# Kernel optimization log

Hardware: AMD Instinct MI355X
Metric: run time of the kernel (lower is better)

The kernel has to match this reference:

```python
import jax, jax.numpy as jnp
import numpy as np

B, N, D, H, FF = 4, 1024, 512, 8, 2048
DH = D // H
RPE_HID = 16
COORD_DIM = 2


def _ln(x, g, b, eps=1e-5):
    m = jnp.mean(x, axis=-1, keepdims=True)
    v = jnp.mean((x - m) ** 2, axis=-1, keepdims=True)
    return (x - m) * jax.lax.rsqrt(v + eps) * g + b


def setup_inputs() -> dict:
    key = jax.random.key(0)
    ks = jax.random.split(key, 20)
    s = 0.02
    inp = {
        "x": jax.random.normal(ks[0], (B, N, D), dtype=jnp.float32),
        "coords": jax.random.uniform(ks[1], (B, N, COORD_DIM), dtype=jnp.float32),
        # qkv + output projections
        "Wq": jax.random.normal(ks[2], (D, D), jnp.float32) * s,
        "bq": jnp.zeros((D,), jnp.float32),
        "Wk": jax.random.normal(ks[3], (D, D), jnp.float32) * s,
        "bk": jnp.zeros((D,), jnp.float32),
        "Wv": jax.random.normal(ks[4], (D, D), jnp.float32) * s,
        "bv": jnp.zeros((D,), jnp.float32),
        "Wo": jax.random.normal(ks[5], (D, D), jnp.float32) * s,
        "bo": jnp.zeros((D,), jnp.float32),
        # learned per-head logit scale (Swin-v2 style cosine attention)
        "logit_scale": jnp.full((H, 1, 1), np.log(10.0), jnp.float32),
        # absolute positional embedder PE: Linear(2 -> D)
        "W_pe": jax.random.normal(ks[6], (COORD_DIM, D), jnp.float32) * s,
        "b_pe": jnp.zeros((D,), jnp.float32),
        # relative positional embedder RPE: MLP(2 -> 16 -> H)
        "W_r1": jax.random.normal(ks[7], (COORD_DIM, RPE_HID), jnp.float32) * 0.5,
        "b_r1": jnp.zeros((RPE_HID,), jnp.float32),
        "W_r2": jax.random.normal(ks[8], (RPE_HID, H), jnp.float32) * 0.5,
        "b_r2": jnp.zeros((H,), jnp.float32),
        # layernorm params
        "g_peq": jnp.ones((D,), jnp.float32), "bt_peq": jnp.zeros((D,), jnp.float32),
        "g_pek": jnp.ones((D,), jnp.float32), "bt_pek": jnp.zeros((D,), jnp.float32),
        "g2": jnp.ones((D,), jnp.float32), "bt2": jnp.zeros((D,), jnp.float32),
        "g3": jnp.ones((D,), jnp.float32), "bt3": jnp.zeros((D,), jnp.float32),
        # MLP (bias=False)
        "W_ff1": jax.random.normal(ks[9], (D, FF), jnp.float32) * s,
        "W_ff2": jax.random.normal(ks[10], (FF, D), jnp.float32) * s,
    }
    return inp


def reference(x, coords, Wq, bq, Wk, bk, Wv, bv, Wo, bo, logit_scale,
              W_pe, b_pe, W_r1, b_r1, W_r2, b_r2,
              g_peq, bt_peq, g_pek, bt_pek, g2, bt2, g3, bt3,
              W_ff1, W_ff2):
    # --- PE add + LayerNorm on q and k (self-attention: coords_cross_ = coords)
    pe = coords @ W_pe + b_pe                      # [B,N,D]
    q = _ln(x + pe, g_peq, bt_peq)
    k = _ln(x + pe, g_pek, bt_pek)
    v = x                                          # v is NOT PE-normed in source

    # --- relative-position bias from cartesian coord differences
    rel = coords[:, :, None, :] - coords[:, None, :, :]   # [B,Nq,Nk,2]
    hid = jax.nn.relu(rel @ W_r1 + b_r1)                  # [B,Nq,Nk,16]
    bias = hid @ W_r2 + b_r2                              # [B,Nq,Nk,H]
    bias = jnp.transpose(bias, (0, 3, 1, 2))              # [B,H,Nq,Nk]

    # --- multi-head cosine attention with learned logit scale
    qp = (q @ Wq + bq).reshape(B, N, H, DH)
    kp = (k @ Wk + bk).reshape(B, N, H, DH)
    vp = (v @ Wv + bv).reshape(B, N, H, DH)
    qn = qp / jnp.maximum(jnp.linalg.norm(qp, axis=-1, keepdims=True), 1e-12)
    kn = kp / jnp.maximum(jnp.linalg.norm(kp, axis=-1, keepdims=True), 1e-12)
    scale = jnp.exp(jnp.minimum(logit_scale, jnp.log(100.0)))  # [H,1,1]
    attn = jnp.einsum('bqhd,bkhd->bhqk', qn, kn) * scale[None] + bias
    attn = jax.nn.softmax(attn, axis=-1)
    att_out = jnp.einsum('bhqk,bkhd->bqhd', attn, vp).reshape(B, N, D)
    att_out = att_out @ Wo + bo

    # --- residual + norm + MLP (LeakyReLU 0.2 after each linear) + residual + norm
    x1 = _ln(x + att_out, g2, bt2)
    mlp = jax.nn.leaky_relu(
        jax.nn.leaky_relu(x1 @ W_ff1, 0.2) @ W_ff2, 0.2)
    return _ln(x1 + mlp, g3, bt3)
```

## Files before the change

### kernel.cpp

```cpp
#include <hip/hip_runtime.h>

#define BB 4
#define NN 1024
#define DD 512
#define HH 8
#define DHH 64
#define FFF 2048

typedef __attribute__((ext_vector_type(8))) short bf16x8;
typedef __attribute__((ext_vector_type(4))) float f32x4;
typedef __attribute__((ext_vector_type(4))) unsigned short u16x4;

__device__ inline float wave_sum(float v) {
#pragma unroll
  for (int off = 32; off; off >>= 1) v += __shfl_xor(v, off);
  return v;
}

__device__ inline unsigned short cvt_bf16(float f) {
  union { float f; unsigned u; } x;
  x.f = f;
  unsigned r = x.u + 0x7FFFu + ((x.u >> 16) & 1u);
  return (unsigned short)(r >> 16);
}

__device__ __forceinline__ void gl_lds16(const void* g, void* l) {
  __builtin_amdgcn_global_load_lds(
      (__attribute__((address_space(1))) void*)(g),
      (__attribute__((address_space(3))) void*)(l), 16, 0, 0);
}

__global__ __launch_bounds__(256) void wconv_kernel(
    const float* __restrict__ W0, const float* __restrict__ W1,
    const float* __restrict__ W2, const float* __restrict__ W3,
    const float* __restrict__ W4, const float* __restrict__ W5,
    unsigned short* __restrict__ out) {
  int bidx = blockIdx.x;
  const float* W; unsigned short* Wt; int K, N, local;
  if (bidx < 256) {
    int sel = bidx >> 6; local = bidx & 63;
    W = sel == 0 ? W0 : sel == 1 ? W1 : sel == 2 ? W2 : W3;
    K = 512; N = 512; Wt = out + (size_t)sel * 262144;
  } else if (bidx < 512) {
    local = bidx - 256; W = W4; K = 512; N = 2048; Wt = out + 1048576;
  } else {
    local = bidx - 512; W = W5; K = 2048; N = 512; Wt = out + 2097152;
  }
  int ntn = N >> 6;
  int tn = (local & (ntn - 1)) << 6, tk = (local / ntn) << 6;
  __shared__ float tile[64][65];
  int tid = threadIdx.x;
#pragma unroll
  for (int i = 0; i < 16; ++i) {
    int e = tid + i * 256, kk = e >> 6, nn = e & 63;
    tile[kk][nn] = W[(size_t)(tk + kk) * N + tn + nn];
  }
  __syncthreads();
#pragma unroll
  for (int i = 0; i < 16; ++i) {
    int e = tid + i * 256, nn = e >> 6, kk = e & 63;
    Wt[(size_t)(tn + nn) * K + tk + kk] = cvt_bf16(tile[kk][nn]);
  }
}

__global__ __launch_bounds__(256) void bias_kernel(
    const float* __restrict__ coords,
    const float* __restrict__ W_r1, const float* __restrict__ b_r1,
    const float* __restrict__ W_r2, const float* __restrict__ b_r2,
    unsigned short* __restrict__ bias_out) {
  int kt = blockIdx.x, qt = blockIdx.y, b = blockIdx.z;
  int tid = threadIdx.x;
  int q = qt * 64 + (tid >> 2);
  int k0 = kt * 32 + (tid & 3) * 8;
  float cq0 = coords[((size_t)b * NN + q) * 2 + 0];
  float cq1 = coords[((size_t)b * NN + q) * 2 + 1];
  float Aq[16];
#pragma unroll
  for (int l = 0; l < 16; ++l)
    Aq[l] = fmaf(cq0, W_r1[l], fmaf(cq1, W_r1[16 + l], b_r1[l]));
  float ck0[8], ck1[8];
#pragma unroll
  for (int kk = 0; kk < 8; ++kk) {
    ck0[kk] = coords[((size_t)b * NN + k0 + kk) * 2 + 0];
    ck1[kk] = coords[((size_t)b * NN + k0 + kk) * 2 + 1];
  }
  float acc[8][8];
#pragma unroll
  for (int kk = 0; kk < 8; ++kk)
#pragma unroll
    for (int h = 0; h < 8; ++h) acc[kk][h] = b_r2[h];
#pragma unroll
  for (int l = 0; l < 16; ++l) {
    float w1a = W_r1[l], w1b = W_r1[16 + l];
#pragma unroll
    for (int kk = 0; kk < 8; ++kk) {
      float hv = Aq[l] - fmaf(ck0[kk], w1a, ck1[kk] * w1b);
      hv = fmaxf(hv, 0.f);
#pragma unroll
      for (int h = 0; h < 8; ++h)
        acc[kk][h] = fmaf(hv, W_r2[l * HH + h], acc[kk][h]);
    }
  }
#pragma unroll
  for (int h = 0; h < 8; ++h) {
    bf16x8 ov;
#pragma unroll
    for (int kk = 0; kk < 8; ++kk) ov[kk] = (short)cvt_bf16(acc[kk][h]);
    *(bf16x8*)&bias_out[(((size_t)b * HH + h) * NN + q) * NN + k0] = ov;
  }
}

__global__ __launch_bounds__(512) void pe_ln_kernel(
    const float* __restrict__ x, const float* __restrict__ coords,
    const float* __restrict__ W_pe, const float* __restrict__ b_pe,
    const float* __restrict__ g_q, const float* __restrict__ bt_q,
    const float* __restrict__ g_k, const float* __restrict__ bt_k,
    unsigned short* __restrict__ q_lnb, unsigned short* __restrict__ k_lnb,
    unsigned short* __restrict__ x_bf) {
  int tid = threadIdx.x;
  int g = tid >> 7, t = tid & 127;
  int row = blockIdx.x * 4 + g;
  int e0 = t * 4;
  float c0 = coords[(size_t)row * 2 + 0];
  float c1 = coords[(size_t)row * 2 + 1];
  size_t base = (size_t)row * DD + e0;
  f32x4 xv = *(const f32x4*)&x[base];
  f32x4 wp0 = *(const f32x4*)&W_pe[e0];
  f32x4 wp1 = *(const f32x4*)&W_pe[DD + e0];
  f32x4 bp  = *(const f32x4*)&b_pe[e0];
  u16x4 xb;
#pragma unroll
  for (int j = 0; j < 4; ++j) xb[j] = cvt_bf16(xv[j]);
  *(u16x4*)&x_bf[base] = xb;
  f32x4 val;
#pragma unroll
  for (int j = 0; j < 4; ++j)
    val[j] = xv[j] + c0 * wp0[j] + c1 * wp1[j] + bp[j];

  __shared__ float ws[8], ws2[8];
  float s = wave_sum(val[0] + val[1] + val[2] + val[3]);
  if ((tid & 63) == 0) ws[tid >> 6] = s;
  __syncthreads();
  float mean = (ws[2 * g] + ws[2 * g + 1]) * (1.f / DD);
  f32x4 dv;
  float s2l = 0.f;
#pragma unroll
  for (int j = 0; j < 4; ++j) { dv[j] = val[j] - mean; s2l = fmaf(dv[j], dv[j], s2l); }
  float s2 = wave_sum(s2l);
  if ((tid & 63) == 0) ws2[tid >> 6] = s2;
  __syncthreads();
  float var = (ws2[2 * g] + ws2[2 * g + 1]) * (1.f / DD);
  float rstd = rsqrtf(var + 1e-5f);
  f32x4 gq = *(const f32x4*)&g_q[e0], bq = *(const f32x4*)&bt_q[e0];
  f32x4 gk = *(const f32x4*)&g_k[e0], bk = *(const f32x4*)&bt_k[e0];
  u16x4 qo, ko;
#pragma unroll
  for (int j = 0; j < 4; ++j) {
    qo[j] = cvt_bf16(dv[j] * rstd * gq[j] + bq[j]);
    ko[j] = cvt_bf16(dv[j] * rstd * gk[j] + bk[j]);
  }
  *(u16x4*)&q_lnb[base] = qo;
  *(u16x4*)&k_lnb[base] = ko;
}

__global__ __launch_bounds__(512) void add_ln_kernel(
    const float* __restrict__ a, const float* __restrict__ r,
    const float* __restrict__ g_, const float* __restrict__ bt,
    float* __restrict__ out, unsigned short* __restrict__ out_bf) {
  int tid = threadIdx.x;
  int g = tid >> 7, t = tid & 127;
  int row = blockIdx.x * 4 + g;
  int e0 = t * 4;
  size_t base = (size_t)row * DD + e0;
  f32x4 av = *(const f32x4*)&a[base];
  f32x4 rv = *(const f32x4*)&r[base];
  f32x4 val;
#pragma unroll
  for (int j = 0; j < 4; ++j) val[j] = av[j] + rv[j];
  __shared__ float ws[8], ws2[8];
  float s = wave_sum(val[0] + val[1] + val[2] + val[3]);
  if ((tid & 63) == 0) ws[tid >> 6] = s;
  __syncthreads();
  float mean = (ws[2 * g] + ws[2 * g + 1]) * (1.f / DD);
  f32x4 dv;
  float s2l = 0.f;
#pragma unroll
  for (int j = 0; j < 4; ++j) { dv[j] = val[j] - mean; s2l = fmaf(dv[j], dv[j], s2l); }
  float s2 = wave_sum(s2l);
  if ((tid & 63) == 0) ws2[tid >> 6] = s2;
  __syncthreads();
  float var = (ws2[2 * g] + ws2[2 * g + 1]) * (1.f / DD);
  float rstd = rsqrtf(var + 1e-5f);
  f32x4 gg = *(const f32x4*)&g_[e0], bb = *(const f32x4*)&bt[e0];
  f32x4 ov;
  u16x4 ob;
#pragma unroll
  for (int j = 0; j < 4; ++j) {
    ov[j] = dv[j] * rstd * gg[j] + bb[j];
    ob[j] = cvt_bf16(ov[j]);
  }
  *(f32x4*)&out[base] = ov;
  if (out_bf) *(u16x4*)&out_bf[base] = ob;
}

template <int ACT, int EPI>
__global__ __launch_bounds__(256) void mgemm_kernel(
    const unsigned short* __restrict__ A, const unsigned short* __restrict__ BT,
    const float* __restrict__ bias, void* __restrict__ C,
    int M, int Nc, int K) {
  __shared__ unsigned short lds[4][8192];
  int tid = threadIdx.x;
  int w = tid >> 6, lane = tid & 63, lg = lane >> 4, lr = lane & 15;
  int bm = blockIdx.y * 128, bn = blockIdx.x * 128;
  int wr = w >> 1, wc = w & 1;
  int segl = lane >> 3;
  int cb = (lane & 7) << 4;

  f32x4 zf = {0.f, 0.f, 0.f, 0.f};
  f32x4 acc[4][4];
#pragma unroll
  for (int mi = 0; mi < 4; ++mi)
#pragma unroll
    for (int ni = 0; ni < 4; ++ni) acc[mi][ni] = zf;

  int nt = K >> 6;

  auto STAGE = [&](int buf, int t) {
    int k0 = t << 6;
#pragma unroll
    for (int i = 0; i < 4; ++i) {
      int seg = w * 4 + i;
      int r = (seg << 3) + segl;
      int csw = cb ^ ((r & 7) << 4);
      const char* ga = (const char*)A + (((size_t)(bm + r) * K + k0) << 1) + csw;
      gl_lds16(ga, &lds[buf * 2][seg << 9]);
      const char* gb = (const char*)BT + (((size_t)(bn + r) * K + k0) << 1) + csw;
      gl_lds16(gb, &lds[buf * 2 + 1][seg << 9]);
    }
  };
  auto COMPUTE = [&](int buf) {
    const unsigned short* As = lds[buf * 2];
    const unsigned short* Bs = lds[buf * 2 + 1];
    bf16x8 af[2][4], bfr[2][4];
#pragma unroll
    for (int kh = 0; kh < 2; ++kh)
#pragma unroll
      for (int mi = 0; mi < 4; ++mi) {
        int r = wr * 64 + mi * 16 + lr;
        int e = (r << 6) + (kh << 5) + (lg << 3);
        af[kh][mi] = *(const bf16x8*)&As[e ^ ((r & 7) << 3)];
        int rb = wc * 64 + mi * 16 + lr;
        int eb = (rb << 6) + (kh << 5) + (lg << 3);
        bfr[kh][mi] = *(const bf16x8*)&Bs[eb ^ ((rb & 7) << 3)];
      }
#pragma unroll
    for (int kh = 0; kh < 2; ++kh)
#pragma unroll
      for (int mi = 0; mi < 4; ++mi)
#pragma unroll
        for (int ni = 0; ni < 4; ++ni)
          acc[mi][ni] = __builtin_amdgcn_mfma_f32_16x16x32_bf16(
// ... 75 lines not shown
        int e = (r << 6) + (kh << 5) + (lg << 3);
        af[kh][mi] = *(const bf16x8*)&As[e ^ ((r & 7) << 3)];
        int rb = wc * 32 + mi * 16 + lr;
        int eb = (rb << 6) + (kh << 5) + (lg << 3);
        bfr[kh][mi] = *(const bf16x8*)&Bs[eb ^ ((rb & 7) << 3)];
      }
#pragma unroll
    for (int kh = 0; kh < 2; ++kh)
#pragma unroll
      for (int mi = 0; mi < 2; ++mi)
#pragma unroll
        for (int ni = 0; ni < 2; ++ni)
          acc[mi][ni] = __builtin_amdgcn_mfma_f32_16x16x32_bf16(
              af[kh][mi], bfr[kh][ni], acc[mi][ni], 0, 0, 0);
  };

  STAGE(0, 0);
  __syncthreads();
  for (int t = 0; t < nt; ++t) {
    if (t + 1 < nt) STAGE((t + 1) & 1, t + 1);
    COMPUTE(t & 1);
    __syncthreads();
  }

#pragma unroll
  for (int ni = 0; ni < 2; ++ni) {
    int col = bn + wc * 32 + ni * 16 + lr;
    float bv = bias ? bias[col] : 0.f;
#pragma unroll
    for (int mi = 0; mi < 2; ++mi) {
#pragma unroll
      for (int j = 0; j < 4; ++j) {
        int row = bm + wr * 32 + mi * 16 + lg * 4 + j;
        float v = acc[mi][ni][j] + bv;
        if (ACT == 1) v = v > 0.f ? v : 0.2f * v;
        if (EPI == 1)
          ((unsigned short*)C)[(size_t)row * Nc + col] = cvt_bf16(v);
        else
          ((float*)C)[(size_t)row * Nc + col] = v;
      }
    }
  }
}

__global__ __launch_bounds__(256) void qkv_gemm_kernel(
    const unsigned short* __restrict__ q_lnb,
    const unsigned short* __restrict__ k_lnb,
    const unsigned short* __restrict__ x_bf,
    const unsigned short* __restrict__ wt,
    const float* __restrict__ bq, const float* __restrict__ bk,
    const float* __restrict__ bv_,
    unsigned short* __restrict__ q_bf, unsigned short* __restrict__ k_bf,
    unsigned short* __restrict__ v_bf) {
  int z = blockIdx.z;
  const unsigned short* A = z == 0 ? q_lnb : z == 1 ? k_lnb : x_bf;
  const unsigned short* BT = wt + (size_t)z * 262144;
  const float* bias = z == 0 ? bq : z == 1 ? bk : bv_;

  __shared__ unsigned short lds[4][8192];
  int tid = threadIdx.x;
  int w = tid >> 6, lane = tid & 63, lg = lane >> 4, lr = lane & 15;
  int bm = blockIdx.y * 128, bn = blockIdx.x * 128;
  int wr = w >> 1, wc = w & 1;
  int segl = lane >> 3;
  int cb = (lane & 7) << 4;

  f32x4 zf = {0.f, 0.f, 0.f, 0.f};
  f32x4 acc[4][4];
#pragma unroll
  for (int mi = 0; mi < 4; ++mi)
#pragma unroll
    for (int ni = 0; ni < 4; ++ni) acc[mi][ni] = zf;

  auto STAGE = [&](int buf, int t) {
    int k0 = t << 6;
#pragma unroll
    for (int i = 0; i < 4; ++i) {
      int seg = w * 4 + i;
      int r = (seg << 3) + segl;
      int csw = cb ^ ((r & 7) << 4);
      const char* ga = (const char*)A + (((size_t)(bm + r) * DD + k0) << 1) + csw;
      gl_lds16(ga, &lds[buf * 2][seg << 9]);
      const char* gb = (const char*)BT + (((size_t)(bn + r) * DD + k0) << 1) + csw;
      gl_lds16(gb, &lds[buf * 2 + 1][seg << 9]);
    }
  };
  auto COMPUTE = [&](int buf) {
    const unsigned short* As = lds[buf * 2];
    const unsigned short* Bs = lds[buf * 2 + 1];
    bf16x8 af[2][4], bfr[2][4];
#pragma unroll
    for (int kh = 0; kh < 2; ++kh)
#pragma unroll
      for (int mi = 0; mi < 4; ++mi) {
        int r = wr * 64 + mi * 16 + lr;
        int e = (r << 6) + (kh << 5) + (lg << 3);
        af[kh][mi] = *(const bf16x8*)&As[e ^ ((r & 7) << 3)];
        int rb = wc * 64 + mi * 16 + lr;
        int eb = (rb << 6) + (kh << 5) + (lg << 3);
        bfr[kh][mi] = *(const bf16x8*)&Bs[eb ^ ((rb & 7) << 3)];
      }
#pragma unroll
    for (int kh = 0; kh < 2; ++kh)
#pragma unroll
      for (int mi = 0; mi < 4; ++mi)
#pragma unroll
        for (int ni = 0; ni < 4; ++ni)
          acc[mi][ni] = __builtin_amdgcn_mfma_f32_16x16x32_bf16(
              af[kh][mi], bfr[kh][ni], acc[mi][ni], 0, 0, 0);
  };

  STAGE(0, 0);
  __syncthreads();
  for (int t = 0; t < 8; ++t) {
    if (t + 1 < 8) STAGE((t + 1) & 1, t + 1);
    COMPUTE(t & 1);
    __syncthreads();
  }

  int h = (bn >> 6) + wc;
  float bvf[4];
#pragma unroll
  for (int ni = 0; ni < 4; ++ni) bvf[ni] = bias[bn + wc * 64 + ni * 16 + lr];
#pragma unroll
  for (int mi = 0; mi < 4; ++mi) {
#pragma unroll
    for (int j = 0; j < 4; ++j) {
      float vals[4]; float ss = 0.f;
#pragma unroll
      for (int ni = 0; ni < 4; ++ni) {
        float v = acc[mi][ni][j] + bvf[ni];
        vals[ni] = v;
        ss = fmaf(v, v, ss);
      }
      float rn = 1.f;
      if (z <= 1) {
        ss += __shfl_xor(ss, 1);
        ss += __shfl_xor(ss, 2);
        ss += __shfl_xor(ss, 4);
        ss += __shfl_xor(ss, 8);
        rn = 1.f / fmaxf(sqrtf(ss), 1e-12f);
      }
      int row = bm + wr * 64 + mi * 16 + lg * 4 + j;
      int b_ = row >> 10, n_ = row & (NN - 1);
      unsigned short* ob = (z == 0 ? q_bf : z == 1 ? k_bf : v_bf) +
                           (((size_t)b_ * HH + h) * NN + n_) * DHH;
#pragma unroll
      for (int ni = 0; ni < 4; ++ni)
        ob[ni * 16 + lr] = cvt_bf16(vals[ni] * rn);
    }
  }
}

__global__ __launch_bounds__(256) void attn_vres_kernel(
    const unsigned short* __restrict__ qb, const unsigned short* __restrict__ kb,
    const unsigned short* __restrict__ vb,
    const unsigned short* __restrict__ bias_g,
    const float* __restrict__ logit_scale,
    unsigned short* __restrict__ part, int nb) {
  const int NT = 4;
  int qt = blockIdx.x, h = blockIdx.y;
  int b = blockIdx.z % nb, sp = blockIdx.z / nb;
  int tid = threadIdx.x;
  int w = tid >> 6, lane = tid & 63;
  int lg = lane >> 4, lr = lane & 15;

  __shared__ unsigned short vt[NT * 4096];
  __shared__ unsigned short pl[4][1024];

  const size_t bh = ((size_t)b * HH + h) * NN;
  const int kt0 = sp * NT;

  int q_glob = qt * 64 + w * 16 + lr;
  bf16x8 aq0 = *(const bf16x8*)&qb[(bh + q_glob) * DHH + lg * 8];
  bf16x8 aq1 = *(const bf16x8*)&qb[(bh + q_glob) * DHH + 32 + lg * 8];

  const unsigned short* brow[4];
#pragma unroll
  for (int r = 0; r < 4; ++r) {
    int qg = qt * 64 + w * 16 + lg * 4 + r;
    brow[r] = &bias_g[(bh + qg) * NN + lr];
  }
  float scale_h = __expf(fminf(logit_scale[h], 4.605170185988091f));

  float m_run[4] = {-1e30f, -1e30f, -1e30f, -1e30f};
  float l_run[4] = {0.f, 0.f, 0.f, 0.f};
  f32x4 zf = {0.f, 0.f, 0.f, 0.f};
  f32x4 acc_o[4] = {zf, zf, zf, zf};

#pragma unroll
  for (int t = 0; t < NT; ++t) {
#pragma unroll
    for (int it = 0; it < 2; ++it) {
      int kl = it * 32 + (tid & 31);
      int d0 = (tid >> 5) * 8;
      bf16x8 vv = *(const bf16x8*)&vb[(bh + (kt0 + t) * 64 + kl) * DHH + d0];
#pragma unroll
      for (int j = 0; j < 8; ++j) {
        int d = d0 + j;
        vt[t * 4096 + ((d * 64 + kl) ^ ((d & 7) << 3))] = (unsigned short)vv[j];
      }
    }
  }
  unsigned short bu[4][4];
#pragma unroll
  for (int r = 0; r < 4; ++r)
#pragma unroll
    for (int kc = 0; kc < 4; ++kc) bu[kc][r] = brow[r][kt0 * 64 + kc * 16];
  __syncthreads();

  for (int t = 0; t < NT; ++t) {
    int ktg = kt0 + t;

    f32x4 s_acc[4];
#pragma unroll
    for (int kc = 0; kc < 4; ++kc) {
      const unsigned short* krow =
          &kb[(bh + ktg * 64 + kc * 16 + lr) * DHH + lg * 8];
      bf16x8 bk0 = *(const bf16x8*)krow;
      bf16x8 bk1 = *(const bf16x8*)(krow + 32);
      s_acc[kc] = __builtin_amdgcn_mfma_f32_16x16x32_bf16(aq0, bk0, zf, 0, 0, 0);
      s_acc[kc] = __builtin_amdgcn_mfma_f32_16x16x32_bf16(aq1, bk1, s_acc[kc], 0, 0, 0);
    }

#pragma unroll
    for (int kc = 0; kc < 4; ++kc)
#pragma unroll
      for (int r = 0; r < 4; ++r) {
        float bf_ = __uint_as_float(((unsigned)bu[kc][r]) << 16);
        s_acc[kc][r] = fmaf(s_acc[kc][r], scale_h, bf_);
      }

    unsigned short bu2[4][4];
    if (t + 1 < NT) {
#pragma unroll
      for (int r = 0; r < 4; ++r)
#pragma unroll
        for (int kc = 0; kc < 4; ++kc)
          bu2[kc][r] = brow[r][(ktg + 1) * 64 + kc * 16];
    }

    float pf[4][4];
#pragma unroll
    for (int r = 0; r < 4; ++r) {
      float mx = fmaxf(fmaxf(s_acc[0][r], s_acc[1][r]),
                       fmaxf(s_acc[2][r], s_acc[3][r]));
      mx = fmaxf(mx, __shfl_xor(mx, 1));
      mx = fmaxf(mx, __shfl_xor(mx, 2));
      mx = fmaxf(mx, __shfl_xor(mx, 4));
      mx = fmaxf(mx, __shfl_xor(mx, 8));
      float m_new = fmaxf(m_run[r], mx);
      float alpha = __expf(m_run[r] - m_new);
      m_run[r] = m_new;
      float ps = 0.f;
#pragma unroll
      for (int kc = 0; kc < 4; ++kc) {
        float p = __expf(s_acc[kc][r] - m_new);
        pf[kc][r] = p;
        ps += p;
      }
      l_run[r] = l_run[r] * alpha + ps;
#pragma unroll
      for (int ds = 0; ds < 4; ++ds) acc_o[ds][r] *= alpha;
    }

#pragma unroll
    for (int kc = 0; kc < 4; ++kc)
#pragma unroll
      for (int r = 0; r < 4; ++r) {
        int q = lg * 4 + r;
        pl[w][(q * 64 + kc * 16 + lr) ^ ((q & 7) << 3)] = cvt_bf16(pf[kc][r]);
      }

#pragma unroll
    for (int ka = 0; ka < 2; ++ka) {
      bf16x8 pa = *(const bf16x8*)&pl[w][(lr * 64 + ka * 32 + lg * 8) ^
                                         ((lr & 7) << 3)];
#pragma unroll
      for (int ds = 0; ds < 4; ++ds) {
        int d = ds * 16 + lr;
        bf16x8 bv = *(const bf16x8*)&vt[t * 4096 +
            ((d * 64 + ka * 32 + lg * 8) ^ ((d & 7) << 3))];
        acc_o[ds] = __builtin_amdgcn_mfma_f32_16x16x32_bf16(pa, bv, acc_o[ds], 0, 0, 0);
      }
    }

    if (t + 1 < NT) {
#pragma unroll
      for (int r = 0; r < 4; ++r)
#pragma unroll
        for (int kc = 0; kc < 4; ++kc) bu[kc][r] = bu2[kc][r];
    }
  }

#pragma unroll
  for (int r = 0; r < 4; ++r) {
    l_run[r] += __shfl_xor(l_run[r], 1);
    l_run[r] += __shfl_xor(l_run[r], 2);
    l_run[r] += __shfl_xor(l_run[r], 4);
    l_run[r] += __shfl_xor(l_run[r], 8);
  }

#pragma unroll
  for (int r = 0; r < 4; ++r) {
    int qg = qt * 64 + w * 16 + lg * 4 + r;
    size_t idx = ((size_t)(sp * nb + b) * HH + h) * NN + qg;
    unsigned short* pr = part + idx * 68;
#pragma unroll
    for (int ds = 0; ds < 4; ++ds)
      pr[ds * 16 + lr] = cvt_bf16(acc_o[ds][r]);
    if (lr == 0) {
      *(float*)(pr + 64) = m_run[r];
      *(float*)(pr + 66) = l_run[r];
    }
  }
}

__global__ __launch_bounds__(256) void attn_kernel1(
    const unsigned short* __restrict__ qb, const unsigned short* __restrict__ kb,
    const unsigned short* __restrict__ vb,
    const unsigned short* __restrict__ bias_g,
    const float* __restrict__ logit_scale,
    unsigned short* __restrict__ attb) {
  int qt = blockIdx.x, h = blockIdx.y, b = blockIdx.z;
  int tid = threadIdx.x;
  int w = tid >> 6, lane = tid & 63;
  int lg = lane >> 4, lr = lane & 15;

  __shared__ unsigned short vt[64 * 64];
  __shared__ unsigned short pl[4][1024];

  const size_t bh = ((size_t)b * HH + h) * NN;

  int q_glob = qt * 64 + w * 16 + lr;
  bf16x8 aq0 = *(const bf16x8*)&qb[(bh + q_glob) * DHH + lg * 8];
  bf16x8 aq1 = *(const bf16x8*)&qb[(bh + q_glob) * DHH + 32 + lg * 8];

  const unsigned short* brow[4];
#pragma unroll
  for (int r = 0; r < 4; ++r) {
    int qg = qt * 64 + w * 16 + lg * 4 + r;
    brow[r] = &bias_g[(bh + qg) * NN + lr];
  }
  float scale_h = __expf(fminf(logit_scale[h], 4.605170185988091f));

  float m_run[4] = {-1e30f, -1e30f, -1e30f, -1e30f};
  float l_run[4] = {0.f, 0.f, 0.f, 0.f};
  f32x4 zf = {0.f, 0.f, 0.f, 0.f};
  f32x4 acc_o[4] = {zf, zf, zf, zf};

  unsigned short bu[4][4];
#pragma unroll
  for (int r = 0; r < 4; ++r)
#pragma unroll
    for (int kc = 0; kc < 4; ++kc) bu[kc][r] = brow[r][kc * 16];

  for (int t = 0; t < 16; ++t) {
    __syncthreads();
#pragma unroll
    for (int it = 0; it < 2; ++it) {
      int kl = it * 32 + (tid & 31);
      int d0 = (tid >> 5) * 8;
      bf16x8 vv = *(const bf16x8*)&vb[(bh + t * 64 + kl) * DHH + d0];
#pragma unroll
      for (int j = 0; j < 8; ++j) {
        int d = d0 + j;
        vt[(d * 64 + kl) ^ ((d & 7) << 3)] = (unsigned short)vv[j];
      }
    }
    __syncthreads();

    f32x4 s_acc[4];
#pragma unroll
    for (int kc = 0; kc < 4; ++kc) {
      const unsigned short* krow =
          &kb[(bh + t * 64 + kc * 16 + lr) * DHH + lg * 8];
      bf16x8 bk0 = *(const bf16x8*)krow;
      bf16x8 bk1 = *(const bf16x8*)(krow + 32);
      s_acc[kc] = __builtin_amdgcn_mfma_f32_16x16x32_bf16(aq0, bk0, zf, 0, 0, 0);
      s_acc[kc] = __builtin_amdgcn_mfma_f32_16x16x32_bf16(aq1, bk1, s_acc[kc], 0, 0, 0);
    }

#pragma unroll
    for (int kc = 0; kc < 4; ++kc)
#pragma unroll
      for (int r = 0; r < 4; ++r) {
        float bf_ = __uint_as_float(((unsigned)bu[kc][r]) << 16);
        s_acc[kc][r] = fmaf(s_acc[kc][r], scale_h, bf_);
      }

    unsigned short bu2[4][4];
    if (t + 1 < 16) {
#pragma unroll
      for (int r = 0; r < 4; ++r)
#pragma unroll
        for (int kc = 0; kc < 4; ++kc)
          bu2[kc][r] = brow[r][(t + 1) * 64 + kc * 16];
    }

    float pf[4][4];
#pragma unroll
    for (int r = 0; r < 4; ++r) {
      float mx = fmaxf(fmaxf(s_acc[0][r], s_acc[1][r]),
                       fmaxf(s_acc[2][r], s_acc[3][r]));
      mx = fmaxf(mx, __shfl_xor(mx, 1));
      mx = fmaxf(mx, __shfl_xor(mx, 2));
      mx = fmaxf(mx, __shfl_xor(mx, 4));
      mx = fmaxf(mx, __shfl_xor(mx, 8));
      float m_new = fmaxf(m_run[r], mx);
      float alpha = __expf(m_run[r] - m_new);
      m_run[r] = m_new;
      float ps = 0.f;
#pragma unroll
      for (int kc = 0; kc < 4; ++kc) {
        float p = __expf(s_acc[kc][r] - m_new);
        pf[kc][r] = p;
        ps += p;
      }
      l_run[r] = l_run[r] * alpha + ps;
#pragma unroll
      for (int ds = 0; ds < 4; ++ds) acc_o[ds][r] *= alpha;
    }

#pragma unroll
    for (int kc = 0; kc < 4; ++kc)
#pragma unroll
      for (int r = 0; r < 4; ++r) {
        int q = lg * 4 + r;
        pl[w][(q * 64 + kc * 16 + lr) ^ ((q & 7) << 3)] = cvt_bf16(pf[kc][r]);
      }

#pragma unroll
    for (int ka = 0; ka < 2; ++ka) {
      bf16x8 pa = *(const bf16x8*)&pl[w][(lr * 64 + ka * 32 + lg * 8) ^
                                         ((lr & 7) << 3)];
#pragma unroll
      for (int ds = 0; ds < 4; ++ds) {
        int d = ds * 16 + lr;
        bf16x8 bv = *(const bf16x8*)&vt[(d * 64 + ka * 32 + lg * 8) ^ ((d & 7) << 3)];
        acc_o[ds] = __builtin_amdgcn_mfma_f32_16x16x32_bf16(pa, bv, acc_o[ds], 0, 0, 0);
      }
    }

    if (t + 1 < 16) {
#pragma unroll
      for (int r = 0; r < 4; ++r)
#pragma unroll
        for (int kc = 0; kc < 4; ++kc) bu[kc][r] = bu2[kc][r];
    }
  }

#pragma unroll
  for (int r = 0; r < 4; ++r) {
    l_run[r] += __shfl_xor(l_run[r], 1);
    l_run[r] += __shfl_xor(l_run[r], 2);
    l_run[r] += __shfl_xor(l_run[r], 4);
    l_run[r] += __shfl_xor(l_run[r], 8);
  }
#pragma unroll
  for (int ds = 0; ds < 4; ++ds)
#pragma unroll
    for (int r = 0; r < 4; ++r) {
      int qg = qt * 64 + w * 16 + lg * 4 + r;
      attb[((size_t)b * NN + qg) * DD + h * DHH + ds * 16 + lr] =
          cvt_bf16(acc_o[ds][r] / l_run[r]);
    }
}

template <int NS>
__global__ __launch_bounds__(256) void combine_kernel(
    const unsigned short* __restrict__ part, unsigned short* __restrict__ attb,
    int nb) {
  int tid = threadIdx.x;
  int w = tid >> 6, d = tid & 63;
  int row = blockIdx.x * 4 + w;
  int b = row >> 13, rem = row & 8191, h = rem >> 10, n = rem & (NN - 1);
  size_t i0 = ((size_t)b * HH + h) * NN + n;
  size_t stride = (size_t)nb * HH * NN;
  float m[NS], l[NS], a[NS];
#pragma unroll
  for (int s = 0; s < NS; ++s) {
    const unsigned short* p = part + (i0 + s * stride) * 68;
    m[s] = *(const float*)(p + 64);
    l[s] = *(const float*)(p + 66);
    a[s] = __uint_as_float(((unsigned)p[d]) << 16);
  }
  float ms = m[0];
#pragma unroll
  for (int s = 1; s < NS; ++s) ms = fmaxf(ms, m[s]);
  float num = 0.f, den = 0.f;
#pragma unroll
  for (int s = 0; s < NS; ++s) {
    float wgt = __expf(m[s] - ms);
    num = fmaf(a[s], wgt, num);
    den = fmaf(l[s], wgt, den);
  }
  attb[((size_t)b * NN + n) * DD + h * DHH + d] = cvt_bf16(num / den);
}

extern "C" void kernel_launch(void* const* d_in, const int* in_sizes, int n_in,
                              void* d_out, int out_size, void* d_ws, size_t ws_size,
                              hipStream_t stream) {
  const float* x      = (const float*)d_in[0];
  const float* coords = (const float*)d_in[1];
  const float* Wq = (const float*)d_in[2];  const float* bq = (const float*)d_in[3];
  const float* Wk = (const float*)d_in[4];  const float* bk = (const float*)d_in[5];
  const float* Wv = (const float*)d_in[6];  const float* bv = (const float*)d_in[7];
  const float* Wo = (const float*)d_in[8];  const float* bo = (const float*)d_in[9];
  const float* logit_scale = (const float*)d_in[10];
  const float* W_pe = (const float*)d_in[11]; const float* b_pe = (const float*)d_in[12];
  const float* W_r1 = (const float*)d_in[13]; const float* b_r1 = (const float*)d_in[14];
  const float* W_r2 = (const float*)d_in[15]; const float* b_r2 = (const float*)d_in[16];
  const float* g_peq = (const float*)d_in[17]; const float* bt_peq = (const float*)d_in[18];
  const float* g_pek = (const float*)d_in[19]; const float* bt_pek = (const float*)d_in[20];
  const float* g2 = (const float*)d_in[21]; const float* bt2 = (const float*)d_in[22];
  const float* g3 = (const float*)d_in[23]; const float* bt3 = (const float*)d_in[24];
  const float* W_ff1 = (const float*)d_in[25];
  const float* W_ff2 = (const float*)d_in[26];
  float* out = (float*)d_out;

  const size_t T = (size_t)BB * NN;
  char* wsb = (char*)d_ws;
  const size_t U = 4u * 1024u * 1024u;

  unsigned short* wt_all = (unsigned short*)(wsb + 0 * U);
  unsigned short* WoT   = wt_all + 786432;
  unsigned short* Wff1T = wt_all + 1048576;
  unsigned short* Wff2T = wt_all + 2097152;
  unsigned short* q_lnb = (unsigned short*)(wsb + 2 * U);
  unsigned short* k_lnb = (unsigned short*)(wsb + 3 * U);
  unsigned short* x_bf  = (unsigned short*)(wsb + 4 * U);
  unsigned short* q_bf  = (unsigned short*)(wsb + 5 * U);
  unsigned short* k_bf  = (unsigned short*)(wsb + 6 * U);
  unsigned short* v_bf  = (unsigned short*)(wsb + 7 * U);
  unsigned short* att_bf = (unsigned short*)(wsb + 8 * U);
  float* proj = (float*)(wsb + 9 * U);
  float* x1   = (float*)(wsb + 11 * U);
  unsigned short* x1_bf = (unsigned short*)(wsb + 13 * U);
  unsigned short* hid_bf = (unsigned short*)(wsb + 2 * U);
  float* mlp  = (float*)(wsb + 9 * U);
  unsigned short* bias_ws = (unsigned short*)(wsb + 9 * U);
  unsigned short* part4_ws = (unsigned short*)(wsb + 25 * U);

  wconv_kernel<<<dim3(768), dim3(256), 0, stream>>>(
      Wq, Wk, Wv, Wo, W_ff1, W_ff2, wt_all);

  pe_ln_kernel<<<dim3(T / 4), dim3(512), 0, stream>>>(
      x, coords, W_pe, b_pe, g_peq, bt_peq, g_pek, bt_pek, q_lnb, k_lnb, x_bf);

  qkv_gemm_kernel<<<dim3(DD / 128, T / 128, 3), dim3(256), 0, stream>>>(
      q_lnb, k_lnb, x_bf, wt_all, bq, bk, bv, q_bf, k_bf, v_bf);

  if (ws_size >= 30 * U) {
    bias_kernel<<<dim3(NN / 32, NN / 64, BB), dim3(256), 0, stream>>>(
        coords, W_r1, b_r1, W_r2, b_r2, bias_ws);
    attn_vres_kernel<<<dim3(NN / 64, HH, 4 * BB), dim3(256), 0, stream>>>(
        q_bf, k_bf, v_bf, bias_ws, logit_scale, part4_ws, BB);
    combine_kernel<4><<<dim3(BB * HH * NN / 4), dim3(256), 0, stream>>>(
        part4_ws, att_bf, BB);
  } else {
    for (int b = 0; b < BB; ++b) {
      bias_kernel<<<dim3(NN / 32, NN / 64, 1), dim3(256), 0, stream>>>(
          coords + (size_t)b * NN * 2, W_r1, b_r1, W_r2, b_r2, bias_ws);
      attn_kernel1<<<dim3(NN / 64, HH, 1), dim3(256), 0, stream>>>(
          q_bf + (size_t)b * HH * NN * DHH, k_bf + (size_t)b * HH * NN * DHH,
          v_bf + (size_t)b * HH * NN * DHH, bias_ws, logit_scale,
          att_bf + (size_t)b * NN * DD);
    }
  }

  mgemm64_kernel<0, 0><<<dim3(DD / 64, T / 64), dim3(256), 0, stream>>>(
      att_bf, WoT, bo, proj, (int)T, DD, DD);

  add_ln_kernel<<<dim3(T / 4), dim3(512), 0, stream>>>(
      x, proj, g2, bt2, x1, x1_bf);

  mgemm_kernel<1, 1><<<dim3(FFF / 128, T / 128), dim3(256), 0, stream>>>(
      x1_bf, Wff1T, nullptr, hid_bf, (int)T, FFF, DD);
  mgemm64_kernel<1, 0><<<dim3(DD / 64, T / 64), dim3(256), 0, stream>>>(
      hid_bf, Wff2T, nullptr, mlp, (int)T, DD, FFF);

  add_ln_kernel<<<dim3(T / 4), dim3(512), 0, stream>>>(
      x1, mlp, g3, bt3, out, nullptr);
}
```

Baseline: 167.0 us.

## Stage attention bias tiles in LDS and split KV across eight partitions

The attention kernel now loads each bias tile with coalesced 16-byte reads into swizzled shared memory, instead of scattered 2-byte per-lane global loads held in registers. NT becomes a template parameter. When the workspace is large enough, the key dimension is split into 8 partitions of 2 tiles each, which doubles the grid size, and an 8-way combine kernel merges the partial results. This trades more partial-result traffic and extra shared memory for higher occupancy and better bias load efficiency.

```diff
diff --git a/kernel.cpp b/kernel.cpp
--- a/kernel.cpp
+++ b/kernel.cpp
@@ -488,13 +488,13 @@
   }
 }
 
+template <int NT>
 __global__ __launch_bounds__(256) void attn_vres_kernel(
     const unsigned short* __restrict__ qb, const unsigned short* __restrict__ kb,
     const unsigned short* __restrict__ vb,
     const unsigned short* __restrict__ bias_g,
     const float* __restrict__ logit_scale,
     unsigned short* __restrict__ part, int nb) {
-  const int NT = 4;
   int qt = blockIdx.x, h = blockIdx.y;
   int b = blockIdx.z % nb, sp = blockIdx.z / nb;
   int tid = threadIdx.x;
@@ -502,6 +502,7 @@
   int lg = lane >> 4, lr = lane & 15;
 
   __shared__ unsigned short vt[NT * 4096];
+  __shared__ unsigned short bl[NT * 4096];
   __shared__ unsigned short pl[4][1024];
 
   const size_t bh = ((size_t)b * HH + h) * NN;
@@ -511,12 +512,6 @@
   bf16x8 aq0 = *(const bf16x8*)&qb[(bh + q_glob) * DHH + lg * 8];
   bf16x8 aq1 = *(const bf16x8*)&qb[(bh + q_glob) * DHH + 32 + lg * 8];
 
-  const unsigned short* brow[4];
-#pragma unroll
-  for (int r = 0; r < 4; ++r) {
-    int qg = qt * 64 + w * 16 + lg * 4 + r;
-    brow[r] = &bias_g[(bh + qg) * NN + lr];
-  }
   float scale_h = __expf(fminf(logit_scale[h], 4.605170185988091f));
 
   float m_run[4] = {-1e30f, -1e30f, -1e30f, -1e30f};
@@ -527,6 +522,14 @@
 #pragma unroll
   for (int t = 0; t < NT; ++t) {
 #pragma unroll
+    for (int i = 0; i < 2; ++i) {
+      int idx = i * 256 + tid;
+      int q = idx >> 3, chunk = idx & 7;
+      bf16x8 bv = *(const bf16x8*)&bias_g[(bh + qt * 64 + q) * NN +
+                                          (kt0 + t) * 64 + chunk * 8];
+      *(bf16x8*)&bl[t * 4096 + q * 64 + ((chunk ^ (q & 7)) << 3)] = bv;
+    }
+#pragma unroll
     for (int it = 0; it < 2; ++it) {
       int kl = it * 32 + (tid & 31);
       int d0 = (tid >> 5) * 8;
@@ -538,11 +541,6 @@
       }
     }
   }
-  unsigned short bu[4][4];
-#pragma unroll
-  for (int r = 0; r < 4; ++r)
-#pragma unroll
-    for (int kc = 0; kc < 4; ++kc) bu[kc][r] = brow[r][kt0 * 64 + kc * 16];
   __syncthreads();
 
   for (int t = 0; t < NT; ++t) {
@@ -563,18 +561,12 @@
     for (int kc = 0; kc < 4; ++kc)
 #pragma unroll
       for (int r = 0; r < 4; ++r) {
-        float bf_ = __uint_as_float(((unsigned)bu[kc][r]) << 16);
+        int q = w * 16 + lg * 4 + r;
+        unsigned short ub =
+            bl[t * 4096 + q * 64 + ((kc * 16 + lr) ^ ((q & 7) << 3))];
+        float bf_ = __uint_as_float(((unsigned)ub) << 16);
         s_acc[kc][r] = fmaf(s_acc[kc][r], scale_h, bf_);
       }
-
-    unsigned short bu2[4][4];
-    if (t + 1 < NT) {
-#pragma unroll
-      for (int r = 0; r < 4; ++r)
-#pragma unroll
-        for (int kc = 0; kc < 4; ++kc)
-          bu2[kc][r] = brow[r][(ktg + 1) * 64 + kc * 16];
-    }
 
     float pf[4][4];
 #pragma unroll
@@ -619,13 +611,6 @@
             ((d * 64 + ka * 32 + lg * 8) ^ ((d & 7) << 3))];
         acc_o[ds] = __builtin_amdgcn_mfma_f32_16x16x32_bf16(pa, bv, acc_o[ds], 0, 0, 0);
       }
-    }
-
-    if (t + 1 < NT) {
-#pragma unroll
-      for (int r = 0; r < 4; ++r)
-#pragma unroll
-        for (int kc = 0; kc < 4; ++kc) bu[kc][r] = bu2[kc][r];
     }
   }
 
@@ -876,7 +861,7 @@
   unsigned short* hid_bf = (unsigned short*)(wsb + 2 * U);
   float* mlp  = (float*)(wsb + 9 * U);
   unsigned short* bias_ws = (unsigned short*)(wsb + 9 * U);
-  unsigned short* part4_ws = (unsigned short*)(wsb + 25 * U);
+  unsigned short* part_ws = (unsigned short*)(wsb + 25 * U);
 
   wconv_kernel<<<dim3(768), dim3(256), 0, stream>>>(
       Wq, Wk, Wv, Wo, W_ff1, W_ff2, wt_all);
@@ -887,13 +872,20 @@
   qkv_gemm_kernel<<<dim3(DD / 128, T / 128, 3), dim3(256), 0, stream>>>(
       q_lnb, k_lnb, x_bf, wt_all, bq, bk, bv, q_bf, k_bf, v_bf);
 
-  if (ws_size >= 30 * U) {
+  if (ws_size >= 34 * U) {
     bias_kernel<<<dim3(NN / 32, NN / 64, BB), dim3(256), 0, stream>>>(
         coords, W_r1, b_r1, W_r2, b_r2, bias_ws);
-    attn_vres_kernel<<<dim3(NN / 64, HH, 4 * BB), dim3(256), 0, stream>>>(
-        q_bf, k_bf, v_bf, bias_ws, logit_scale, part4_ws, BB);
+    attn_vres_kernel<2><<<dim3(NN / 64, HH, 8 * BB), dim3(256), 0, stream>>>(
+        q_bf, k_bf, v_bf, bias_ws, logit_scale, part_ws, BB);
+    combine_kernel<8><<<dim3(BB * HH * NN / 4), dim3(256), 0, stream>>>(
+        part_ws, att_bf, BB);
+  } else if (ws_size >= 30 * U) {
+    bias_kernel<<<dim3(NN / 32, NN / 64, BB), dim3(256), 0, stream>>>(
+        coords, W_r1, b_r1, W_r2, b_r2, bias_ws);
+    attn_vres_kernel<4><<<dim3(NN / 64, HH, 4 * BB), dim3(256), 0, stream>>>(
+        q_bf, k_bf, v_bf, bias_ws, logit_scale, part_ws, BB);
     combine_kernel<4><<<dim3(BB * HH * NN / 4), dim3(256), 0, stream>>>(
-        part4_ws, att_bf, BB);
+        part_ws, att_bf, BB);
   } else {
     for (int b = 0; b < BB; ++b) {
       bias_kernel<<<dim3(NN / 32, NN / 64, 1), dim3(256), 0, stream>>>(
```

Result: slower. 175.7 us (+5.2%).

## Replace online softmax with precomputed static row-max upper bound

Applied to the files above, without the earlier changes.

The bias kernel now also writes per-row, per-tile maxima of the relative-position bias. The attention kernel uses them to form a fixed upper bound on each row's logits (bias max plus the cosine-scale bound), so it can drop the running max, the rescale factors and the cross-lane max reductions. The combine kernel then simply sums partial numerators and denominators without exponential reweighting. This adds an extra rowmax buffer and reads, and relies on the bound being tight enough to avoid underflow in exp.

```diff
diff --git a/kernel.cpp b/kernel.cpp
--- a/kernel.cpp
+++ b/kernel.cpp
@@ -67,7 +67,7 @@
     const float* __restrict__ coords,
     const float* __restrict__ W_r1, const float* __restrict__ b_r1,
     const float* __restrict__ W_r2, const float* __restrict__ b_r2,
-    unsigned short* __restrict__ bias_out) {
+    unsigned short* __restrict__ bias_out, float* __restrict__ rowmax_out) {
   int kt = blockIdx.x, qt = blockIdx.y, b = blockIdx.z;
   int tid = threadIdx.x;
   int q = qt * 64 + (tid >> 2);
@@ -101,12 +101,24 @@
         acc[kk][h] = fmaf(hv, W_r2[l * HH + h], acc[kk][h]);
     }
   }
+  float mk[8];
 #pragma unroll
   for (int h = 0; h < 8; ++h) {
+    float m = acc[0][h];
+#pragma unroll
+    for (int kk = 1; kk < 8; ++kk) m = fmaxf(m, acc[kk][h]);
+    m = fmaxf(m, __shfl_xor(m, 1));
+    m = fmaxf(m, __shfl_xor(m, 2));
+    mk[h] = m;
     bf16x8 ov;
 #pragma unroll
     for (int kk = 0; kk < 8; ++kk) ov[kk] = (short)cvt_bf16(acc[kk][h]);
     *(bf16x8*)&bias_out[(((size_t)b * HH + h) * NN + q) * NN + k0] = ov;
+  }
+  if ((tid & 3) == 0) {
+#pragma unroll
+    for (int h = 0; h < 8; ++h)
+      rowmax_out[(((size_t)b * HH + h) * NN + q) * 32 + kt] = mk[h];
   }
 }
 
@@ -488,13 +500,14 @@
   }
 }
 
+template <int NT>
 __global__ __launch_bounds__(256) void attn_vres_kernel(
     const unsigned short* __restrict__ qb, const unsigned short* __restrict__ kb,
     const unsigned short* __restrict__ vb,
     const unsigned short* __restrict__ bias_g,
+    const float* __restrict__ rowmax_g,
     const float* __restrict__ logit_scale,
     unsigned short* __restrict__ part, int nb) {
-  const int NT = 4;
   int qt = blockIdx.x, h = blockIdx.y;
   int b = blockIdx.z % nb, sp = blockIdx.z / nb;
   int tid = threadIdx.x;
@@ -512,14 +525,22 @@
   bf16x8 aq1 = *(const bf16x8*)&qb[(bh + q_glob) * DHH + 32 + lg * 8];
 
   const unsigned short* brow[4];
+  float m_ub[4];
+  float scale_h = __expf(fminf(logit_scale[h], 4.605170185988091f));
 #pragma unroll
   for (int r = 0; r < 4; ++r) {
     int qg = qt * 64 + w * 16 + lg * 4 + r;
     brow[r] = &bias_g[(bh + qg) * NN + lr];
-  }
-  float scale_h = __expf(fminf(logit_scale[h], 4.605170185988091f));
-
-  float m_run[4] = {-1e30f, -1e30f, -1e30f, -1e30f};
+    const float* rmp = &rowmax_g[(bh + qg) * 32];
+    float rm = -1e30f;
+#pragma unroll
+    for (int i = 0; i < 8; ++i) {
+      f32x4 v = *(const f32x4*)&rmp[i * 4];
+      rm = fmaxf(rm, fmaxf(fmaxf(v[0], v[1]), fmaxf(v[2], v[3])));
+    }
+    m_ub[r] = rm + 1.05f * scale_h + 0.1f;
+  }
+
   float l_run[4] = {0.f, 0.f, 0.f, 0.f};
   f32x4 zf = {0.f, 0.f, 0.f, 0.f};
   f32x4 acc_o[4] = {zf, zf, zf, zf};
@@ -559,6 +580,132 @@
       s_acc[kc] = __builtin_amdgcn_mfma_f32_16x16x32_bf16(aq1, bk1, s_acc[kc], 0, 0, 0);
     }
 
+    unsigned short bu2[4][4];
+    if (t + 1 < NT) {
+#pragma unroll
+      for (int r = 0; r < 4; ++r)
+#pragma unroll
+        for (int kc = 0; kc < 4; ++kc)
+          bu2[kc][r] = brow[r][(ktg + 1) * 64 + kc * 16];
+    }
+
+#pragma unroll
+    for (int kc = 0; kc < 4; ++kc)
+#pragma unroll
+      for (int r = 0; r < 4; ++r) {
+        float bf_ = __uint_as_float(((unsigned)bu[kc][r]) << 16);
+        float p = __expf(fmaf(s_acc[kc][r], scale_h, bf_ - m_ub[r]));
+        l_run[r] += p;
+        int q = lg * 4 + r;
+        pl[w][(q * 64 + kc * 16 + lr) ^ ((q & 7) << 3)] = cvt_bf16(p);
+      }
+
+#pragma unroll
+    for (int ka = 0; ka < 2; ++ka) {
+      bf16x8 pa = *(const bf16x8*)&pl[w][(lr * 64 + ka * 32 + lg * 8) ^
+                                         ((lr & 7) << 3)];
+#pragma unroll
+      for (int ds = 0; ds < 4; ++ds) {
+        int d = ds * 16 + lr;
+        bf16x8 bv = *(const bf16x8*)&vt[t * 4096 +
+            ((d * 64 + ka * 32 + lg * 8) ^ ((d & 7) << 3))];
+        acc_o[ds] = __builtin_amdgcn_mfma_f32_16x16x32_bf16(pa, bv, acc_o[ds], 0, 0, 0);
+      }
+    }
+
+    if (t + 1 < NT) {
+#pragma unroll
+      for (int r = 0; r < 4; ++r)
+#pragma unroll
+        for (int kc = 0; kc < 4; ++kc) bu[kc][r] = bu2[kc][r];
+    }
+  }
+
+#pragma unroll
+  for (int r = 0; r < 4; ++r) {
+    l_run[r] += __shfl_xor(l_run[r], 1);
+    l_run[r] += __shfl_xor(l_run[r], 2);
+    l_run[r] += __shfl_xor(l_run[r], 4);
+    l_run[r] += __shfl_xor(l_run[r], 8);
+  }
+
+#pragma unroll
+  for (int r = 0; r < 4; ++r) {
+    int qg = qt * 64 + w * 16 + lg * 4 + r;
+    size_t idx = ((size_t)(sp * nb + b) * HH + h) * NN + qg;
+    unsigned short* pr = part + idx * 68;
+#pragma unroll
+    for (int ds = 0; ds < 4; ++ds)
+      pr[ds * 16 + lr] = cvt_bf16(acc_o[ds][r]);
+    if (lr == 0) *(float*)(pr + 64) = l_run[r];
+  }
+}
+
+__global__ __launch_bounds__(256) void attn_kernel1(
+    const unsigned short* __restrict__ qb, const unsigned short* __restrict__ kb,
+    const unsigned short* __restrict__ vb,
+    const unsigned short* __restrict__ bias_g,
+    const float* __restrict__ logit_scale,
+    unsigned short* __restrict__ attb) {
+  int qt = blockIdx.x, h = blockIdx.y, b = blockIdx.z;
+  int tid = threadIdx.x;
+  int w = tid >> 6, lane = tid & 63;
+  int lg = lane >> 4, lr = lane & 15;
+
+  __shared__ unsigned short vt[64 * 64];
+  __shared__ unsigned short pl[4][1024];
+
+  const size_t bh = ((size_t)b * HH + h) * NN;
+
+  int q_glob = qt * 64 + w * 16 + lr;
+  bf16x8 aq0 = *(const bf16x8*)&qb[(bh + q_glob) * DHH + lg * 8];
+  bf16x8 aq1 = *(const bf16x8*)&qb[(bh + q_glob) * DHH + 32 + lg * 8];
+
+  const unsigned short* brow[4];
+#pragma unroll
+  for (int r = 0; r < 4; ++r) {
+    int qg = qt * 64 + w * 16 + lg * 4 + r;
+    brow[r] = &bias_g[(bh + qg) * NN + lr];
+  }
+  float scale_h = __expf(fminf(logit_scale[h], 4.605170185988091f));
+
+  float m_run[4] = {-1e30f, -1e30f, -1e30f, -1e30f};
+  float l_run[4] = {0.f, 0.f, 0.f, 0.f};
+  f32x4 zf = {0.f, 0.f, 0.f, 0.f};
+  f32x4 acc_o[4] = {zf, zf, zf, zf};
+
+  unsigned short bu[4][4];
+#pragma unroll
+  for (int r = 0; r < 4; ++r)
+#pragma unroll
+    for (int kc = 0; kc < 4; ++kc) bu[kc][r] = brow[r][kc * 16];
+
+  for (int t = 0; t < 16; ++t) {
+    __syncthreads();
+#pragma unroll
+    for (int it = 0; it < 2; ++it) {
+      int kl = it * 32 + (tid & 31);
+      int d0 = (tid >> 5) * 8;
+      bf16x8 vv = *(const bf16x8*)&vb[(bh + t * 64 + kl) * DHH + d0];
+#pragma unroll
+      for (int j = 0; j < 8; ++j) {
+        int d = d0 + j;
+        vt[(d * 64 + kl) ^ ((d & 7) << 3)] = (unsigned short)vv[j];
+      }
+    }
+    __syncthreads();
+
+    f32x4 s_acc[4];
+#pragma unroll
+    for (int kc = 0; kc < 4; ++kc) {
+      const unsigned short* krow =
+          &kb[(bh + t * 64 + kc * 16 + lr) * DHH + lg * 8];
+      bf16x8 bk0 = *(const bf16x8*)krow;
+      bf16x8 bk1 = *(const bf16x8*)(krow + 32);
+      s_acc[kc] = __builtin_amdgcn_mfma_f32_16x16x32_bf16(aq0, bk0, zf, 0, 0, 0);
+      s_acc[kc] = __builtin_amdgcn_mfma_f32_16x16x32_bf16(aq1, bk1, s_acc[kc], 0, 0, 0);
+    }
+
 #pragma unroll
     for (int kc = 0; kc < 4; ++kc)
 #pragma unroll
@@ -568,12 +715,12 @@
       }
 
     unsigned short bu2[4][4];
-    if (t + 1 < NT) {
+    if (t + 1 < 16) {
 #pragma unroll
       for (int r = 0; r < 4; ++r)
 #pragma unroll
         for (int kc = 0; kc < 4; ++kc)
-          bu2[kc][r] = brow[r][(ktg + 1) * 64 + kc * 16];
+          bu2[kc][r] = brow[r][(t + 1) * 64 + kc * 16];
     }
 
     float pf[4][4];
@@ -615,164 +762,6 @@
 #pragma unroll
       for (int ds = 0; ds < 4; ++ds) {
         int d = ds * 16 + lr;
-        bf16x8 bv = *(const bf16x8*)&vt[t * 4096 +
-            ((d * 64 + ka * 32 + lg * 8) ^ ((d & 7) << 3))];
-        acc_o[ds] = __builtin_amdgcn_mfma_f32_16x16x32_bf16(pa, bv, acc_o[ds], 0, 0, 0);
-      }
-    }
-
-    if (t + 1 < NT) {
-#pragma unroll
-      for (int r = 0; r < 4; ++r)
-#pragma unroll
-        for (int kc = 0; kc < 4; ++kc) bu[kc][r] = bu2[kc][r];
-    }
-  }
-
-#pragma unroll
-  for (int r = 0; r < 4; ++r) {
-    l_run[r] += __shfl_xor(l_run[r], 1);
-    l_run[r] += __shfl_xor(l_run[r], 2);
-    l_run[r] += __shfl_xor(l_run[r], 4);
-    l_run[r] += __shfl_xor(l_run[r], 8);
-  }
-
-#pragma unroll
-  for (int r = 0; r < 4; ++r) {
-    int qg = qt * 64 + w * 16 + lg * 4 + r;
-    size_t idx = ((size_t)(sp * nb + b) * HH + h) * NN + qg;
-    unsigned short* pr = part + idx * 68;
-#pragma unroll
-    for (int ds = 0; ds < 4; ++ds)
-      pr[ds * 16 + lr] = cvt_bf16(acc_o[ds][r]);
-    if (lr == 0) {
-      *(float*)(pr + 64) = m_run[r];
-      *(float*)(pr + 66) = l_run[r];
-    }
-  }
-}
-
-__global__ __launch_bounds__(256) void attn_kernel1(
-    const unsigned short* __restrict__ qb, const unsigned short* __restrict__ kb,
-    const unsigned short* __restrict__ vb,
-    const unsigned short* __restrict__ bias_g,
-    const float* __restrict__ logit_scale,
-    unsigned short* __restrict__ attb) {
-  int qt = blockIdx.x, h = blockIdx.y, b = blockIdx.z;
-  int tid = threadIdx.x;
-  int w = tid >> 6, lane = tid & 63;
-  int lg = lane >> 4, lr = lane & 15;
-
-  __shared__ unsigned short vt[64 * 64];
-  __shared__ unsigned short pl[4][1024];
-
-  const size_t bh = ((size_t)b * HH + h) * NN;
-
-  int q_glob = qt * 64 + w * 16 + lr;
-  bf16x8 aq0 = *(const bf16x8*)&qb[(bh + q_glob) * DHH + lg * 8];
-  bf16x8 aq1 = *(const bf16x8*)&qb[(bh + q_glob) * DHH + 32 + lg * 8];
-
-  const unsigned short* brow[4];
-#pragma unroll
-  for (int r = 0; r < 4; ++r) {
-    int qg = qt * 64 + w * 16 + lg * 4 + r;
-    brow[r] = &bias_g[(bh + qg) * NN + lr];
-  }
-  float scale_h = __expf(fminf(logit_scale[h], 4.605170185988091f));
-
-  float m_run[4] = {-1e30f, -1e30f, -1e30f, -1e30f};
-  float l_run[4] = {0.f, 0.f, 0.f, 0.f};
-  f32x4 zf = {0.f, 0.f, 0.f, 0.f};
-  f32x4 acc_o[4] = {zf, zf, zf, zf};
-
-  unsigned short bu[4][4];
-#pragma unroll
-  for (int r = 0; r < 4; ++r)
-#pragma unroll
-    for (int kc = 0; kc < 4; ++kc) bu[kc][r] = brow[r][kc * 16];
-
-  for (int t = 0; t < 16; ++t) {
-    __syncthreads();
-#pragma unroll
-    for (int it = 0; it < 2; ++it) {
-      int kl = it * 32 + (tid & 31);
-      int d0 = (tid >> 5) * 8;
-      bf16x8 vv = *(const bf16x8*)&vb[(bh + t * 64 + kl) * DHH + d0];
-#pragma unroll
-      for (int j = 0; j < 8; ++j) {
-        int d = d0 + j;
-        vt[(d * 64 + kl) ^ ((d & 7) << 3)] = (unsigned short)vv[j];
-      }
-    }
-    __syncthreads();
-
-    f32x4 s_acc[4];
-#pragma unroll
-    for (int kc = 0; kc < 4; ++kc) {
-      const unsigned short* krow =
-          &kb[(bh + t * 64 + kc * 16 + lr) * DHH + lg * 8];
-      bf16x8 bk0 = *(const bf16x8*)krow;
-      bf16x8 bk1 = *(const bf16x8*)(krow + 32);
-      s_acc[kc] = __builtin_amdgcn_mfma_f32_16x16x32_bf16(aq0, bk0, zf, 0, 0, 0);
-      s_acc[kc] = __builtin_amdgcn_mfma_f32_16x16x32_bf16(aq1, bk1, s_acc[kc], 0, 0, 0);
-    }
-
-#pragma unroll
-    for (int kc = 0; kc < 4; ++kc)
-#pragma unroll
-      for (int r = 0; r < 4; ++r) {
-        float bf_ = __uint_as_float(((unsigned)bu[kc][r]) << 16);
-        s_acc[kc][r] = fmaf(s_acc[kc][r], scale_h, bf_);
-      }
-
-    unsigned short bu2[4][4];
-    if (t + 1 < 16) {
-#pragma unroll
-      for (int r = 0; r < 4; ++r)
-#pragma unroll
-        for (int kc = 0; kc < 4; ++kc)
-          bu2[kc][r] = brow[r][(t + 1) * 64 + kc * 16];
-    }
-
-    float pf[4][4];
-#pragma unroll
-    for (int r = 0; r < 4; ++r) {
-      float mx = fmaxf(fmaxf(s_acc[0][r], s_acc[1][r]),
-                       fmaxf(s_acc[2][r], s_acc[3][r]));
-      mx = fmaxf(mx, __shfl_xor(mx, 1));
-      mx = fmaxf(mx, __shfl_xor(mx, 2));
-      mx = fmaxf(mx, __shfl_xor(mx, 4));
-      mx = fmaxf(mx, __shfl_xor(mx, 8));
-      float m_new = fmaxf(m_run[r], mx);
-      float alpha = __expf(m_run[r] - m_new);
-      m_run[r] = m_new;
-      float ps = 0.f;
-#pragma unroll
-      for (int kc = 0; kc < 4; ++kc) {
-        float p = __expf(s_acc[kc][r] - m_new);
-        pf[kc][r] = p;
-        ps += p;
-      }
-      l_run[r] = l_run[r] * alpha + ps;
-#pragma unroll
-      for (int ds = 0; ds < 4; ++ds) acc_o[ds][r] *= alpha;
-    }
-
-#pragma unroll
-    for (int kc = 0; kc < 4; ++kc)
-#pragma unroll
-      for (int r = 0; r < 4; ++r) {
-        int q = lg * 4 + r;
-        pl[w][(q * 64 + kc * 16 + lr) ^ ((q & 7) << 3)] = cvt_bf16(pf[kc][r]);
-      }
-
-#pragma unroll
-    for (int ka = 0; ka < 2; ++ka) {
-      bf16x8 pa = *(const bf16x8*)&pl[w][(lr * 64 + ka * 32 + lg * 8) ^
-                                         ((lr & 7) << 3)];
-#pragma unroll
-      for (int ds = 0; ds < 4; ++ds) {
-        int d = ds * 16 + lr;
         bf16x8 bv = *(const bf16x8*)&vt[(d * 64 + ka * 32 + lg * 8) ^ ((d & 7) << 3)];
         acc_o[ds] = __builtin_amdgcn_mfma_f32_16x16x32_bf16(pa, bv, acc_o[ds], 0, 0, 0);
       }
@@ -813,23 +802,12 @@
   int b = row >> 13, rem = row & 8191, h = rem >> 10, n = rem & (NN - 1);
   size_t i0 = ((size_t)b * HH + h) * NN + n;
   size_t stride = (size_t)nb * HH * NN;
-  float m[NS], l[NS], a[NS];
+  float num = 0.f, den = 0.f;
 #pragma unroll
   for (int s = 0; s < NS; ++s) {
     const unsigned short* p = part + (i0 + s * stride) * 68;
-    m[s] = *(const float*)(p + 64);
-    l[s] = *(const float*)(p + 66);
-    a[s] = __uint_as_float(((unsigned)p[d]) << 16);
-  }
-  float ms = m[0];
-#pragma unroll
-  for (int s = 1; s < NS; ++s) ms = fmaxf(ms, m[s]);
-  float num = 0.f, den = 0.f;
-#pragma unroll
-  for (int s = 0; s < NS; ++s) {
-    float wgt = __expf(m[s] - ms);
-    num = fmaf(a[s], wgt, num);
-    den = fmaf(l[s], wgt, den);
+    num += __uint_as_float(((unsigned)p[d]) << 16);
+    den += *(const float*)(p + 64);
   }
   attb[((size_t)b * NN + n) * DD + h * DHH + d] = cvt_bf16(num / den);
 }
@@ -876,7 +854,8 @@
   unsigned short* hid_bf = (unsigned short*)(wsb + 2 * U);
   float* mlp  = (float*)(wsb + 9 * U);
   unsigned short* bias_ws = (unsigned short*)(wsb + 9 * U);
-  unsigned short* part4_ws = (unsigned short*)(wsb + 25 * U);
+  unsigned short* part_ws = (unsigned short*)(wsb + 25 * U);
+  float* rowmax_ws = (float*)(wsb + 30 * U);
 
   wconv_kernel<<<dim3(768), dim3(256), 0, stream>>>(
       Wq, Wk, Wv, Wo, W_ff1, W_ff2, wt_all);
@@ -887,17 +866,20 @@
   qkv_gemm_kernel<<<dim3(DD / 128, T / 128, 3), dim3(256), 0, stream>>>(
       q_lnb, k_lnb, x_bf, wt_all, bq, bk, bv, q_bf, k_bf, v_bf);
 
-  if (ws_size >= 30 * U) {
+  if (ws_size >= 31 * U) {
     bias_kernel<<<dim3(NN / 32, NN / 64, BB), dim3(256), 0, stream>>>(
-        coords, W_r1, b_r1, W_r2, b_r2, bias_ws);
-    attn_vres_kernel<<<dim3(NN / 64, HH, 4 * BB), dim3(256), 0, stream>>>(
-        q_bf, k_bf, v_bf, bias_ws, logit_scale, part4_ws, BB);
+        coords, W_r1, b_r1, W_r2, b_r2, bias_ws, rowmax_ws);
+    attn_vres_kernel<4><<<dim3(NN / 64, HH, 4 * BB), dim3(256), 0, stream>>>(
+        q_bf, k_bf, v_bf, bias_ws, rowmax_ws, logit_scale, part_ws, BB);
     combine_kernel<4><<<dim3(BB * HH * NN / 4), dim3(256), 0, stream>>>(
-        part4_ws, att_bf, BB);
+        part_ws, att_bf, BB);
   } else {
+    float* rm_b = (float*)(wsb + 13 * U);
+    (void)rm_b;
     for (int b = 0; b < BB; ++b) {
       bias_kernel<<<dim3(NN / 32, NN / 64, 1), dim3(256), 0, stream>>>(
-          coords + (size_t)b * NN * 2, W_r1, b_r1, W_r2, b_r2, bias_ws);
+          coords + (size_t)b * NN * 2, W_r1, b_r1, W_r2, b_r2, bias_ws,
+          (float*)(wsb + 13 * U));
       attn_kernel1<<<dim3(NN / 64, HH, 1), dim3(256), 0, stream>>>(
           q_bf + (size_t)b * HH * NN * DHH, k_bf + (size_t)b * HH * NN * DHH,
           v_bf + (size_t)b * HH * NN * DHH, bias_ws, logit_scale,
```

New measurement: 170.2 us. About the same (+1.9%).
